# Kernel optimization log

Measured on AMD Instinct MI355X. Metric: run time of the kernel, lower is better.

The kernel has to match this reference:

```python
import jax, jax.numpy as jnp
import numpy as np

N_FFT = 1024
N_STAGES = 3
N_SUB = N_FFT >> N_STAGES  # 128 = base IDFT size
BATCH = 32768


def quant8(x):
    # fake-quantize to int8 with power-of-2 scale (matches torch quant8)
    mv = jnp.max(jnp.abs(x))
    q = jnp.ceil(jnp.log2(mv)) - 6.0
    s = jnp.exp2(q)
    return jnp.round(x / s) * s


def idft_mats(n):
    # inverse DFT matrix: W[n,k] = exp(+2*pi*i*n*k/N) / N (symmetric)
    k = np.arange(n)
    ang = 2.0 * np.pi * np.outer(k, k) / n
    wr = (np.cos(ang) / n).astype(np.float32)
    wi = (np.sin(ang) / n).astype(np.float32)
    return jnp.asarray(wr), jnp.asarray(wi)


def bitrev(n_bits):
    idx = np.arange(1 << n_bits)
    rev = np.zeros_like(idx)
    for b in range(n_bits):
        rev |= ((idx >> b) & 1) << (n_bits - 1 - b)
    return rev


def setup_inputs() -> dict:
    key = jax.random.key(0)
    k1, k2 = jax.random.split(key)
    re = jax.random.normal(k1, (BATCH, N_FFT), jnp.float32)
    im = jax.random.normal(k2, (BATCH, N_FFT), jnp.float32)
    wr, wi = idft_mats(N_SUB)
    wr_u = quant8(wr)
    wi_u = quant8(wi)
    return {
        "re": re, "im": im,
        "wr_u": wr_u, "wr_l": wr - wr_u,
        "wi_u": wi_u, "wi_l": wi - wi_u,
    }


def _v16_matmul(x, wu, wl):
    # Virtual16bMatmul: split-precision matmul, upper + lower parts
    return x @ wu.T + x @ wl.T


def reference(re, im, wr_u, wr_l, wi_u, wi_l):
    B = re.shape[0]
    S = 1 << N_STAGES
    order = bitrev(N_STAGES)  # static numpy permutation

    # FFTPermuter: perms[j] = x[..., bitrev(j)::S] -> [S, B, N_SUB]
    def perm(x):
        return jnp.transpose(x.reshape(B, N_SUB, S)[..., order], (2, 0, 1))

    rp = perm(re)
    ip = perm(im)

    # IDFTv2 on all 2^n_stages sub-sequences at once (batched matmul)
    yr = _v16_matmul(rp, wr_u, wr_l) - _v16_matmul(ip, wi_u, wi_l)
    yi = _v16_matmul(rp, wi_u, wi_l) + _v16_matmul(ip, wr_u, wr_l)

    # FFTwiddle stages: consecutive blocks pair as (even, odd)
    L = N_SUB
    for _ in range(N_STAGES):
        er, ei = yr[0::2], yi[0::2]   # [M/2, B, L]
        orr, oi = yr[1::2], yi[1::2]
        k = jnp.arange(L, dtype=jnp.float32)
        ang = 2.0 * jnp.pi * k / jnp.float32(2 * L)
        tr, ti = jnp.cos(ang), jnp.sin(ang)  # inverse twiddles e^{+2pi i k/(2L)}
        pr = tr * orr - ti * oi
        pi = tr * oi + ti * orr
        yr = jnp.concatenate([er + pr, er - pr], axis=-1)  # [M/2, B, 2L]
        yi = jnp.concatenate([ei + pi, ei - pi], axis=-1)
        L *= 2

    # IFFTNormalizer: divide by 2^n_stages (total scale 1/n_fft)
    scale = jnp.float32(1.0 / (1 << N_STAGES))
    return yr[0] * scale, yi[0] * scale
```

## Files before the change

### kernel.cpp

```cpp
#include <hip/hip_runtime.h>
#include <math.h>


#define BATCH_N   32768
#define NFFT      1024
#define TB        16
#define NTHREADS  1024
#define GRID_N    (BATCH_N / TB)

typedef __attribute__((ext_vector_type(8))) short  short8;
typedef __attribute__((ext_vector_type(4))) float  floatx4;

#define W_STRIDE   136
#define W_PLANE    (128 * W_STRIDE)
#define A_STRIDE   136
#define A_PLANE    (128 * A_STRIDE)
#define Y_STRIDE   130
#define OFF_W      0
#define OFF_A      (2 * W_PLANE * 2)
#define OFF_TW     (OFF_A + 2 * A_PLANE * 2)
#define SMEM_BYTES (OFF_TW + 1024 * 8)

__device__ __forceinline__ unsigned short f2bf(float f) {
    unsigned u = __float_as_uint(f);
    u += 0x7fffu + ((u >> 16) & 1u);
    return (unsigned short)(u >> 16);
}
__device__ __forceinline__ float bf2f(unsigned v) {
    return __uint_as_float(v << 16);
}
__device__ __forceinline__ short8 negbf(short8 a) {
    union { short8 s; unsigned u[4]; } x;
    x.s = a;
    x.u[0] ^= 0x80008000u; x.u[1] ^= 0x80008000u;
    x.u[2] ^= 0x80008000u; x.u[3] ^= 0x80008000u;
    return x.s;
}

__global__ __launch_bounds__(NTHREADS, 1)
void ifft_fused(const float* __restrict__ re, const float* __restrict__ im,
                const float* __restrict__ wru, const float* __restrict__ wrl,
                const float* __restrict__ wiu, const float* __restrict__ wil,
                float* __restrict__ out)
{
    extern __shared__ char smem[];
    unsigned short* Wr = (unsigned short*)(smem + OFF_W);
    unsigned short* Wi = Wr + W_PLANE;
    unsigned short* Ar = (unsigned short*)(smem + OFF_A);
    unsigned short* Ai = Ar + A_PLANE;
    unsigned*       Y  = (unsigned*)(smem + OFF_A);
    float2*         TW = (float2*)(smem + OFF_TW);

    const int t   = threadIdx.x;
    const int blk = blockIdx.x;

#pragma unroll
    for (int i = 0; i < 4; ++i) {
        int e   = (t + NTHREADS * i) * 4;
        int row = e >> 7, col = e & 127;
        float4 a = *(const float4*)(wru + e);
        float4 b = *(const float4*)(wrl + e);
        ushort4 pk;
        pk.x = f2bf(a.x + b.x); pk.y = f2bf(a.y + b.y);
        pk.z = f2bf(a.z + b.z); pk.w = f2bf(a.w + b.w);
        *(ushort4*)(Wr + row * W_STRIDE + col) = pk;
        a = *(const float4*)(wiu + e);
        b = *(const float4*)(wil + e);
        pk.x = f2bf(a.x + b.x); pk.y = f2bf(a.y + b.y);
        pk.z = f2bf(a.z + b.z); pk.w = f2bf(a.w + b.w);
        *(ushort4*)(Wi + row * W_STRIDE + col) = pk;
    }

    {
        float ang = 6.2831853071795864769f * (1.0f / 1024.0f) * (float)t;
        float s, c;
        __sincosf(ang, &s, &c);
        TW[t] = make_float2(c * 0.125f, s * 0.125f);
    }

#pragma unroll
    for (int i = 0; i < 8; ++i) {
        int e    = (t + NTHREADS * i) * 4;
        int isIm = (e >= TB * NFFT);
        int er   = e & (TB * NFFT - 1);
        int b    = er >> 10;
        int p    = er & 1023;
        const float* src = isIm ? im : re;
        float4 v = *(const float4*)(src + (size_t)(blk * TB + b) * NFFT + p);
        unsigned short* plane = isIm ? Ai : Ar;
        int r0 = p & 7, col = p >> 3;
        int base = (b * 8 + r0) * A_STRIDE + col;
        plane[base + 0 * A_STRIDE] = f2bf(v.x);
        plane[base + 1 * A_STRIDE] = f2bf(v.y);
        plane[base + 2 * A_STRIDE] = f2bf(v.z);
        plane[base + 3 * A_STRIDE] = f2bf(v.w);
    }

    __syncthreads();

    const int w    = t >> 6;
    const int lane = t & 63;
    const int wm   = w & 3;
    const int wn   = w >> 2;
    const int l15  = lane & 15, quad = lane >> 4;

    floatx4 accr[2][2] = {};
    floatx4 acci[2][2] = {};

#pragma unroll
    for (int ks = 0; ks < 4; ++ks) {
        const int kk = ks * 32 + quad * 8;
        short8 arf[2], aif[2], ainf[2], wrf[2], wif[2];
#pragma unroll
        for (int tm = 0; tm < 2; ++tm) {
            int row = (wm * 2 + tm) * 16 + l15;
            arf[tm]  = *(const short8*)(Ar + row * A_STRIDE + kk);
            aif[tm]  = *(const short8*)(Ai + row * A_STRIDE + kk);
            ainf[tm] = negbf(aif[tm]);
        }
#pragma unroll
        for (int tn = 0; tn < 2; ++tn) {
            int rowW = (wn * 2 + tn) * 16 + l15;
            wrf[tn] = *(const short8*)(Wr + rowW * W_STRIDE + kk);
            wif[tn] = *(const short8*)(Wi + rowW * W_STRIDE + kk);
        }
#pragma unroll
        for (int tm = 0; tm < 2; ++tm)
#pragma unroll
            for (int tn = 0; tn < 2; ++tn) {
                accr[tm][tn] = __builtin_amdgcn_mfma_f32_16x16x32_bf16(arf[tm],  wrf[tn], accr[tm][tn], 0, 0, 0);
                accr[tm][tn] = __builtin_amdgcn_mfma_f32_16x16x32_bf16(ainf[tm], wif[tn], accr[tm][tn], 0, 0, 0);
                acci[tm][tn] = __builtin_amdgcn_mfma_f32_16x16x32_bf16(arf[tm],  wif[tn], acci[tm][tn], 0, 0, 0);
                acci[tm][tn] = __builtin_amdgcn_mfma_f32_16x16x32_bf16(aif[tm],  wrf[tn], acci[tm][tn], 0, 0, 0);
            }
    }

    __syncthreads();

#pragma unroll
    for (int tm = 0; tm < 2; ++tm)
#pragma unroll
        for (int tn = 0; tn < 2; ++tn)
#pragma unroll
            for (int rg = 0; rg < 4; ++rg) {
                int row = (wm * 2 + tm) * 16 + quad * 4 + rg;
                int col = (wn * 2 + tn) * 16 + l15;
                unsigned pr = f2bf(accr[tm][tn][rg]);
                unsigned pi = f2bf(acci[tm][tn][rg]);
                Y[row * Y_STRIDE + col] = pr | (pi << 16);
            }

    __syncthreads();

    const int m0 = t & 63;
    const int bl = t >> 6;
    float u_re[2][8], u_im[2][8];

#pragma unroll
    for (int half = 0; half < 2; ++half) {
        int m = 2 * m0 + half;
        float zr[8], zi[8];
#pragma unroll
        for (int r = 0; r < 8; ++r) {
            unsigned pk = Y[(bl * 8 + r) * Y_STRIDE + m];
            float yre = bf2f(pk & 0xffffu);
            float yim = bf2f(pk >> 16);
            float2 tw = TW[r * m];
            zr[r] = tw.x * yre - tw.y * yim;
            zi[r] = tw.x * yim + tw.y * yre;
        }
        float t0r = zr[0] + zr[4], t0i = zi[0] + zi[4];
        float t1r = zr[0] - zr[4], t1i = zi[0] - zi[4];
        float t2r = zr[2] + zr[6], t2i = zi[2] + zi[6];
        float t3r = zr[2] - zr[6], t3i = zi[2] - zi[6];
        float E0r = t0r + t2r, E0i = t0i + t2i;
        float E2r = t0r - t2r, E2i = t0i - t2i;
        float E1r = t1r - t3i, E1i = t1i + t3r;
        float E3r = t1r + t3i, E3i = t1i - t3r;
        float s0r = zr[1] + zr[5], s0i = zi[1] + zi[5];
        float s1r = zr[1] - zr[5], s1i = zi[1] - zi[5];
        float s2r = zr[3] + zr[7], s2i = zi[3] + zi[7];
        float s3r = zr[3] - zr[7], s3i = zi[3] - zi[7];
        float O0r = s0r + s2r, O0i = s0i + s2i;
        float O2r = s0r - s2r, O2i = s0i - s2i;
        float O1r = s1r - s3i, O1i = s1i + s3r;
        float O3r = s1r + s3i, O3i = s1i - s3r;
        const float C8 = 0.70710678118654752f;
        float p0r = O0r,                  p0i = O0i;
        float p1r = C8 * (O1r - O1i),     p1i = C8 * (O1r + O1i);
        float p2r = -O2i,                 p2i = O2r;
        float p3r = -C8 * (O3r + O3i),    p3i = C8 * (O3r - O3i);
        u_re[half][0] = E0r + p0r; u_im[half][0] = E0i + p0i;
        u_re[half][1] = E1r + p1r; u_im[half][1] = E1i + p1i;
        u_re[half][2] = E2r + p2r; u_im[half][2] = E2i + p2i;
        u_re[half][3] = E3r + p3r; u_im[half][3] = E3i + p3i;
        u_re[half][4] = E0r - p0r; u_im[half][4] = E0i - p0i;
        u_re[half][5] = E1r - p1r; u_im[half][5] = E1i - p1i;
        u_re[half][6] = E2r - p2r; u_im[half][6] = E2i - p2i;
        u_re[half][7] = E3r - p3r; u_im[half][7] = E3i - p3i;
    }

    {
        size_t bg = (size_t)(blk * TB + bl);
        float* outre = out + bg * NFFT + 2 * m0;
        float* outim = out + (size_t)BATCH_N * NFFT + bg * NFFT + 2 * m0;
#pragma unroll
        for (int q = 0; q < 8; ++q) {
            *(float2*)(outre + q * 128) = make_float2(u_re[0][q], u_re[1][q]);
            *(float2*)(outim + q * 128) = make_float2(u_im[0][q], u_im[1][q]);
        }
    }
}

extern "C" void kernel_launch(void* const* d_in, const int* in_sizes, int n_in,
                              void* d_out, int out_size, void* d_ws, size_t ws_size,
                              hipStream_t stream) {
    const float* re  = (const float*)d_in[0];
    const float* im  = (const float*)d_in[1];
    const float* wru = (const float*)d_in[2];
    const float* wrl = (const float*)d_in[3];
    const float* wiu = (const float*)d_in[4];
    const float* wil = (const float*)d_in[5];
    float* out = (float*)d_out;

    static bool attr_set = false;
    (void)hipFuncSetAttribute((const void*)ifft_fused,
                              hipFuncAttributeMaxDynamicSharedMemorySize, SMEM_BYTES);

    ifft_fused<<<GRID_N, NTHREADS, SMEM_BYTES, stream>>>(re, im, wru, wrl, wiu, wil, out);
}
```

Before: 469.6 us.

## Precompute bf16 twiddle matrix in workspace, shrink blocks, compute twiddles in registers

A small prep kernel now converts the split W matrices to scaled bf16 once into workspace, and the main kernel reads W fragments straight from global memory instead of staging them in LDS on every block. The block shrinks to 8 batch rows and 512 threads with launch bounds allowing 4 blocks per CU, which cuts LDS to about 35 KB per block so several blocks can be resident. Twiddles are computed in registers by recurrence from one sincos instead of an LDS table, and Y reads are vectorized as uint2. This trades repeated per-block W conversion and LDS pressure for global/L2 W loads and an extra kernel launch, with the 1/8 scale moved into W.

```diff
diff --git a/kernel.cpp b/kernel.cpp
--- a/kernel.cpp
+++ b/kernel.cpp
@@ -4,22 +4,17 @@
 
 #define BATCH_N   32768
 #define NFFT      1024
-#define TB        16
-#define NTHREADS  1024
+#define TB        8
+#define NTHREADS  512
 #define GRID_N    (BATCH_N / TB)
 
 typedef __attribute__((ext_vector_type(8))) short  short8;
 typedef __attribute__((ext_vector_type(4))) float  floatx4;
 
-#define W_STRIDE   136
-#define W_PLANE    (128 * W_STRIDE)
 #define A_STRIDE   136
-#define A_PLANE    (128 * A_STRIDE)
+#define A_PLANE    (64 * A_STRIDE)
 #define Y_STRIDE   130
-#define OFF_W      0
-#define OFF_A      (2 * W_PLANE * 2)
-#define OFF_TW     (OFF_A + 2 * A_PLANE * 2)
-#define SMEM_BYTES (OFF_TW + 1024 * 8)
+#define SMEM_BYTES (2 * A_PLANE * 2)
 
 __device__ __forceinline__ unsigned short f2bf(float f) {
     unsigned u = __float_as_uint(f);
@@ -37,46 +32,36 @@
     return x.s;
 }
 
-__global__ __launch_bounds__(NTHREADS, 1)
+__global__ void prep_w(const float* __restrict__ wru, const float* __restrict__ wrl,
+                       const float* __restrict__ wiu, const float* __restrict__ wil,
+                       unsigned short* __restrict__ wbf)
+{
+    int e = (blockIdx.x * 256 + threadIdx.x) * 4;
+    float4 a = *(const float4*)(wru + e);
+    float4 b = *(const float4*)(wrl + e);
+    ushort4 pk;
+    pk.x = f2bf((a.x + b.x) * 0.125f); pk.y = f2bf((a.y + b.y) * 0.125f);
+    pk.z = f2bf((a.z + b.z) * 0.125f); pk.w = f2bf((a.w + b.w) * 0.125f);
+    *(ushort4*)(wbf + e) = pk;
+    a = *(const float4*)(wiu + e);
+    b = *(const float4*)(wil + e);
+    pk.x = f2bf((a.x + b.x) * 0.125f); pk.y = f2bf((a.y + b.y) * 0.125f);
+    pk.z = f2bf((a.z + b.z) * 0.125f); pk.w = f2bf((a.w + b.w) * 0.125f);
+    *(ushort4*)(wbf + 16384 + e) = pk;
+}
+
+__global__ __launch_bounds__(NTHREADS, 4)
 void ifft_fused(const float* __restrict__ re, const float* __restrict__ im,
-                const float* __restrict__ wru, const float* __restrict__ wrl,
-                const float* __restrict__ wiu, const float* __restrict__ wil,
+                const unsigned short* __restrict__ wbf,
                 float* __restrict__ out)
 {
-    extern __shared__ char smem[];
-    unsigned short* Wr = (unsigned short*)(smem + OFF_W);
-    unsigned short* Wi = Wr + W_PLANE;
-    unsigned short* Ar = (unsigned short*)(smem + OFF_A);
+    __shared__ __align__(16) char smem[SMEM_BYTES];
+    unsigned short* Ar = (unsigned short*)smem;
     unsigned short* Ai = Ar + A_PLANE;
-    unsigned*       Y  = (unsigned*)(smem + OFF_A);
-    float2*         TW = (float2*)(smem + OFF_TW);
+    unsigned*       Y  = (unsigned*)smem;
 
     const int t   = threadIdx.x;
     const int blk = blockIdx.x;
-
-#pragma unroll
-    for (int i = 0; i < 4; ++i) {
-        int e   = (t + NTHREADS * i) * 4;
-        int row = e >> 7, col = e & 127;
-        float4 a = *(const float4*)(wru + e);
-        float4 b = *(const float4*)(wrl + e);
-        ushort4 pk;
-        pk.x = f2bf(a.x + b.x); pk.y = f2bf(a.y + b.y);
-        pk.z = f2bf(a.z + b.z); pk.w = f2bf(a.w + b.w);
-        *(ushort4*)(Wr + row * W_STRIDE + col) = pk;
-        a = *(const float4*)(wiu + e);
-        b = *(const float4*)(wil + e);
-        pk.x = f2bf(a.x + b.x); pk.y = f2bf(a.y + b.y);
-        pk.z = f2bf(a.z + b.z); pk.w = f2bf(a.w + b.w);
-        *(ushort4*)(Wi + row * W_STRIDE + col) = pk;
-    }
-
-    {
-        float ang = 6.2831853071795864769f * (1.0f / 1024.0f) * (float)t;
-        float s, c;
-        __sincosf(ang, &s, &c);
-        TW[t] = make_float2(c * 0.125f, s * 0.125f);
-    }
 
 #pragma unroll
     for (int i = 0; i < 8; ++i) {
@@ -95,14 +80,15 @@
         plane[base + 2 * A_STRIDE] = f2bf(v.z);
         plane[base + 3 * A_STRIDE] = f2bf(v.w);
     }
-
     __syncthreads();
 
     const int w    = t >> 6;
     const int lane = t & 63;
-    const int wm   = w & 3;
-    const int wn   = w >> 2;
+    const int wm   = w & 1;
+    const int wn   = w >> 1;
     const int l15  = lane & 15, quad = lane >> 4;
+    const unsigned short* Wrg = wbf;
+    const unsigned short* Wig = wbf + 16384;
 
     floatx4 accr[2][2] = {};
     floatx4 acci[2][2] = {};
@@ -121,8 +107,8 @@
 #pragma unroll
         for (int tn = 0; tn < 2; ++tn) {
             int rowW = (wn * 2 + tn) * 16 + l15;
-            wrf[tn] = *(const short8*)(Wr + rowW * W_STRIDE + kk);
-            wif[tn] = *(const short8*)(Wi + rowW * W_STRIDE + kk);
+            wrf[tn] = *(const short8*)(Wrg + rowW * 128 + kk);
+            wif[tn] = *(const short8*)(Wig + rowW * 128 + kk);
         }
 #pragma unroll
         for (int tm = 0; tm < 2; ++tm)
@@ -154,20 +140,34 @@
 
     const int m0 = t & 63;
     const int bl = t >> 6;
+
+    uint2 zpk[8];
+#pragma unroll
+    for (int r = 0; r < 8; ++r)
+        zpk[r] = *(const uint2*)(Y + (bl * 8 + r) * Y_STRIDE + 2 * m0);
+
     float u_re[2][8], u_im[2][8];
 
 #pragma unroll
     for (int half = 0; half < 2; ++half) {
         int m = 2 * m0 + half;
+        float cr[8], sr[8];
+        cr[0] = 1.0f; sr[0] = 0.0f;
+        __sincosf((float)m * 6.135923151542565e-3f, &sr[1], &cr[1]);
+#pragma unroll
+        for (int r = 2; r < 8; ++r) {
+            int ha = r >> 1, hb = r - ha;
+            cr[r] = cr[ha] * cr[hb] - sr[ha] * sr[hb];
+            sr[r] = cr[ha] * sr[hb] + sr[ha] * cr[hb];
+        }
         float zr[8], zi[8];
 #pragma unroll
         for (int r = 0; r < 8; ++r) {
-            unsigned pk = Y[(bl * 8 + r) * Y_STRIDE + m];
+            unsigned pk = half ? zpk[r].y : zpk[r].x;
             float yre = bf2f(pk & 0xffffu);
             float yim = bf2f(pk >> 16);
-            float2 tw = TW[r * m];
-            zr[r] = tw.x * yre - tw.y * yim;
-            zi[r] = tw.x * yim + tw.y * yre;
+            zr[r] = cr[r] * yre - sr[r] * yim;
+            zi[r] = cr[r] * yim + sr[r] * yre;
         }
         float t0r = zr[0] + zr[4], t0i = zi[0] + zi[4];
         float t1r = zr[0] - zr[4], t1i = zi[0] - zi[4];
@@ -217,15 +217,9 @@
                               hipStream_t stream) {
     const float* re  = (const float*)d_in[0];
     const float* im  = (const float*)d_in[1];
-    const float* wru = (const float*)d_in[2];
-    const float* wrl = (const float*)d_in[3];
-    const float* wiu = (const float*)d_in[4];
-    const float* wil = (const float*)d_in[5];
-    float* out = (float*)d_out;
-
-    static bool attr_set = false;
-    (void)hipFuncSetAttribute((const void*)ifft_fused,
-                              hipFuncAttributeMaxDynamicSharedMemorySize, SMEM_BYTES);
-
-    ifft_fused<<<GRID_N, NTHREADS, SMEM_BYTES, stream>>>(re, im, wru, wrl, wiu, wil, out);
-}
+    unsigned short* wbf = (unsigned short*)d_ws;
+
+    prep_w<<<16, 256, 0, stream>>>((const float*)d_in[2], (const float*)d_in[3],
+                                   (const float*)d_in[4], (const float*)d_in[5], wbf);
+    ifft_fused<<<GRID_N, NTHREADS, 0, stream>>>(re, im, wbf, (float*)d_out);
+}
```

New measurement: 466.6 us. About the same (-0.6%).
